# Performance work log

Measured on AMD Instinct MI355X. Metric: run time of the kernel, lower is better.

## Reference

```python
import jax, jax.numpy as jnp
import numpy as np


def setup_inputs() -> dict:
    key = jax.random.key(0)
    k1, k2 = jax.random.split(key)
    queries = jax.random.normal(k1, (8, 4096, 512), dtype=jnp.float32)
    items = jax.random.normal(k2, (1024, 512), dtype=jnp.float32)
    return {"queries": queries, "items": items}


def reference(queries, items):
    # queries: (B, S, F), items: (K, F); reduction='none', memto_framework=True
    # Phase-only (unit magnitude) reconstruction along the sequence axis.
    f = jnp.fft.rfft(queries, axis=1)                     # (B, S//2+1, F) complex64
    unit = jnp.fft.irfft(jnp.exp(-1j * jnp.angle(f)), axis=1)  # (B, S, F) float32 (S even)
    # Dense score against shared memory, then top-1 nearest memory item.
    score = jnp.einsum('bsf,kf->bsk', unit, items)        # (B, S, K)
    idx = jnp.argmax(score, axis=-1)                      # (B, S) int, top-1 index
    step_basis = items[idx]                               # gather -> (B, S, F)
    # MSE with reduction='none' is elementwise squared error; then sum over features.
    gathering_loss = jnp.sum((queries - step_basis) ** 2, axis=-1)  # (B, S)
    return gathering_loss
```

## Files before the change

### kernel.cpp

```cpp
#include <hip/hip_runtime.h>


#define NB 8
#define NS 4096
#define NF 512
#define NK 1024
#define NROWS (NB * NS)
#define NKB 8
#define KK 1024

#define SWZF(i) ((i) ^ (((i) >> 4) & 15))

typedef _Float16 half8 __attribute__((ext_vector_type(8)));
typedef float floatx4 __attribute__((ext_vector_type(4)));
struct H2 { _Float16 x, y; };

__device__ __forceinline__ float2 cmulf(float2 a, float2 b) {
    return make_float2(a.x * b.x - a.y * b.y, a.x * b.y + a.y * b.x);
}

__device__ __forceinline__ float2 unitize(float2 v) {
    float m2 = v.x * v.x + v.y * v.y;
    if (m2 > 0.f) {
        float inv = 1.0f / sqrtf(m2);
        return make_float2(v.x * inv, v.y * inv);
    }
    return make_float2(1.f, 0.f);
}

__device__ __forceinline__ H2 split_h2(float v) {
    _Float16 h = (_Float16)v;
    float lo = v - (float)h;
    H2 r; r.x = h; r.y = (_Float16)lo; return r;
}

__device__ __forceinline__ void dft4(float2 a, float2 b, float2 c, float2 d,
                                     float2& o0, float2& o1, float2& o2, float2& o3) {
    float2 apc = make_float2(a.x + c.x, a.y + c.y);
    float2 amc = make_float2(a.x - c.x, a.y - c.y);
    float2 bpd = make_float2(b.x + d.x, b.y + d.y);
    float2 bmd = make_float2(b.x - d.x, b.y - d.y);
    o0 = make_float2(apc.x + bpd.x, apc.y + bpd.y);
    o1 = make_float2(amc.x + bmd.y, amc.y - bmd.x);
    o2 = make_float2(apc.x - bpd.x, apc.y - bpd.y);
    o3 = make_float2(amc.x - bmd.y, amc.y + bmd.x);
}

__global__ void twiddle_init(float2* __restrict__ W) {
    int k = blockIdx.x * 256 + threadIdx.x;
    double ang = -2.0 * 3.14159265358979323846 * (double)k / 4096.0;
    W[k] = make_float2((float)cos(ang), (float)sin(ang));
}

__global__ __launch_bounds__(256) void transpose_kernel(
        const float* __restrict__ q, float* __restrict__ qt) {
    __shared__ float tile[32][33];
    int b = blockIdx.z;
    int s0 = blockIdx.x * 32;
    int f0 = blockIdx.y * 32;
    int tx = threadIdx.x;
    int ty = threadIdx.y;
    const float* qb = q + (size_t)b * NS * NF;
    float* qtb = qt + (size_t)b * NF * NS;
#pragma unroll
    for (int i = 0; i < 4; ++i) {
        int s = s0 + ty + i * 8;
        tile[ty + i * 8][tx] = qb[(size_t)s * NF + f0 + tx];
    }
    __syncthreads();
#pragma unroll
    for (int i = 0; i < 4; ++i) {
        int f = f0 + ty + i * 8;
        qtb[(size_t)f * NS + s0 + tx] = tile[tx][ty + i * 8];
    }
}

__device__ __forceinline__ void fft4096_r16(float2* A, float2* B,
                                            const float2* __restrict__ W, int t) {
    const float C1 = 0.92387953251128674f;
    const float S1 = 0.38268343236508978f;
    const float R2 = 0.70710678118654752f;
    const float2 w1 = make_float2(C1, -S1);
    const float2 w2 = make_float2(R2, -R2);
    const float2 w3 = make_float2(S1, -C1);
    const float2 w4 = make_float2(0.f, -1.f);
    const float2 w6 = make_float2(-R2, -R2);
    const float2 w9 = make_float2(-C1, S1);
#pragma unroll
    for (int st = 0; st < 3; ++st) {
        float2* src = (st == 1) ? B : A;
        float2* dst = (st == 1) ? A : B;
        const int s = (st == 0) ? 1 : (st == 1) ? 16 : 256;
        __syncthreads();
        float2 x[16];
#pragma unroll
        for (int j = 0; j < 16; ++j) x[j] = src[SWZF(t + j * 256)];
        float2 y[4][4];
#pragma unroll
        for (int n0 = 0; n0 < 4; ++n0)
            dft4(x[n0], x[4 + n0], x[8 + n0], x[12 + n0],
                 y[n0][0], y[n0][1], y[n0][2], y[n0][3]);
        y[1][1] = cmulf(w1, y[1][1]);
        y[1][2] = cmulf(w2, y[1][2]);
        y[1][3] = cmulf(w3, y[1][3]);
        y[2][1] = cmulf(w2, y[2][1]);
        y[2][2] = cmulf(w4, y[2][2]);
        y[2][3] = cmulf(w6, y[2][3]);
        y[3][1] = cmulf(w3, y[3][1]);
        y[3][2] = cmulf(w6, y[3][2]);
        y[3][3] = cmulf(w9, y[3][3]);
        float2 z[16];
#pragma unroll
        for (int k0 = 0; k0 < 4; ++k0)
            dft4(y[0][k0], y[1][k0], y[2][k0], y[3][k0],
                 z[k0], z[4 + k0], z[8 + k0], z[12 + k0]);
        const int q = t & (s - 1);
        const int pw = t - q;
        const int dbase = 16 * t - 15 * q;
        dst[SWZF(dbase)] = z[0];
        if (st == 2) {
#pragma unroll
            for (int j = 1; j < 16; ++j)
                dst[SWZF(dbase + j * s)] = z[j];
        } else {
#pragma unroll
            for (int j = 1; j < 16; ++j)
                dst[SWZF(dbase + j * s)] = cmulf(W[(j * pw) & 4095], z[j]);
        }
    }
}

__global__ __launch_bounds__(256) void fft_phase_kernel(
        const float* __restrict__ qt, H2* __restrict__ u2,
        const float2* __restrict__ W) {
    __shared__ float2 bufA[4096];
    __shared__ float2 bufB[4096];
    const int t = threadIdx.x;
    const float* x0 = qt + (size_t)(2 * blockIdx.x) * NS;
    const float* x1 = x0 + NS;

    const float4* a4 = (const float4*)x0;
    const float4* b4 = (const float4*)x1;
#pragma unroll
    for (int i = 0; i < 4; ++i) {
        int idx = t + i * 256;
        float4 va = a4[idx];
        float4 vb = b4[idx];
        bufA[SWZF(idx * 4 + 0)] = make_float2(va.x, vb.x);
        bufA[SWZF(idx * 4 + 1)] = make_float2(va.y, vb.y);
        bufA[SWZF(idx * 4 + 2)] = make_float2(va.z, vb.z);
        bufA[SWZF(idx * 4 + 3)] = make_float2(va.w, vb.w);
    }

    fft4096_r16(bufA, bufB, W, t);
    __syncthreads();

#pragma unroll
    for (int j = 0; j < 8; ++j) {
        int k = t + j * 256;
        if (k == 0) {
            float2 z0 = bufB[SWZF(0)];
            float2 zh = bufB[SWZF(2048)];
            float2 u00 = unitize(make_float2(z0.x, 0.f));
            float2 u10 = unitize(make_float2(z0.y, 0.f));
            bufB[SWZF(0)] = make_float2(u00.x, u10.x);
            float2 u0h = unitize(make_float2(zh.x, 0.f));
            float2 u1h = unitize(make_float2(zh.y, 0.f));
            bufB[SWZF(2048)] = make_float2(u0h.x, u1h.x);
        } else {
            float2 zk = bufB[SWZF(k)];
            float2 zm = bufB[SWZF(4096 - k)];
            float2 a = make_float2(0.5f * (zk.x + zm.x), 0.5f * (zk.y - zm.y));
            float2 bq = make_float2(0.5f * (zk.x - zm.x), 0.5f * (zk.y + zm.y));
            float2 x1k = make_float2(bq.y, -bq.x);
            float2 u0 = unitize(a);
            float2 u1 = unitize(x1k);
            bufB[SWZF(k)] = make_float2(u0.x - u1.y, u0.y + u1.x);
            bufB[SWZF(4096 - k)] = make_float2(u0.x + u1.y, u1.x - u0.y);
        }
    }

    fft4096_r16(bufB, bufA, W, t);
    __syncthreads();

    H2* o0 = u2 + (size_t)(2 * blockIdx.x) * NS;
    H2* o1 = o0 + NS;
    const float c = 0.25f;
#pragma unroll
    for (int i = 0; i < 4; ++i) {
        int idx = t + i * 256;
        H2 t0[4], t1[4];
#pragma unroll
        for (int k = 0; k < 4; ++k) {
            float2 e = bufA[SWZF(idx * 4 + k)];
            t0[k] = split_h2(e.x * c);
            t1[k] = split_h2(e.y * c);
        }
        *(float4*)&o0[idx * 4] = *(float4*)t0;
        *(float4*)&o1[idx * 4] = *(float4*)t1;
    }
}

__global__ __launch_bounds__(256) void abuild_kernel(
        const H2* __restrict__ u2, _Float16* __restrict__ a2) {
    __shared__ H2 tile[64][65];
    const int b = blockIdx.z;
    const int f0 = blockIdx.y * 64;
    const int s0 = blockIdx.x * 64;
    const int t = threadIdx.x;
    const int fr = t >> 6;
    const int sc = t & 63;
#pragma unroll
    for (int i = 0; i < 16; ++i) {
        int f = fr + i * 4;
        tile[f][sc] = u2[(size_t)(b * NF + f0 + f) * NS + s0 + sc];
    }
    __syncthreads();
    const int s = t >> 2;
    const int qd = t & 3;
    _Float16 xs[16], ys[16];
#pragma unroll
    for (int j = 0; j < 16; ++j) {
        H2 v = tile[qd * 16 + j][s];
        xs[j] = v.x;
        ys[j] = v.y;
    }
    size_t rowoff = ((size_t)(b * NS + s0 + s)) * KK;
    _Float16* pr = a2 + rowoff + (f0 + qd * 16);
    *(float4*)&pr[0] = ((float4*)xs)[0];
    *(float4*)&pr[8] = ((float4*)xs)[1];
    _Float16* pl = pr + 512;
    *(float4*)&pl[0] = ((float4*)ys)[0];
    *(float4*)&pl[8] = ((float4*)ys)[1];
}

__global__ __launch_bounds__(256) void bbuild_kernel(
        const float* __restrict__ items, _Float16* __restrict__ b2) {
    int id = blockIdx.x * 256 + threadIdx.x;
    int n = id >> 7, fq = id & 127;
    float4 v = *(const float4*)&items[(size_t)n * NF + fq * 4];
    H2 h0 = split_h2(v.x * 1024.f);
    H2 h1 = split_h2(v.y * 1024.f);
    H2 h2v = split_h2(v.z * 1024.f);
    H2 h3 = split_h2(v.w * 1024.f);
    _Float16 hs[4] = {h0.x, h1.x, h2v.x, h3.x};
    _Float16 ls[4] = {h0.y, h1.y, h2v.y, h3.y};
    _Float16* pr = b2 + (size_t)n * KK + fq * 4;
    *(float2*)pr = *(float2*)hs;
    *(float2*)(pr + 512) = *(float2*)ls;
}

__global__ __launch_bounds__(256, 2) void gemm_mfma_argmax(
        const _Float16* __restrict__ a2, const _Float16* __restrict__ b2,
        float* __restrict__ pbest, int* __restrict__ pidx) {
    __shared__ __align__(16) char smem[2 * 4 * 128 * 64];
    const int sb = blockIdx.x;
    const int kb = blockIdx.y;
    const int row0 = sb * 128;
    const int n0 = kb * 128;
    const int t = threadIdx.x;
    const int wid = t >> 6, l = t & 63, g = l >> 4, c = l & 15;
    const int wr = wid >> 1, wc = wid & 1;

    floatx4 acc[4][4];
#pragma unroll
    for (int m = 0; m < 4; ++m)
#pragma unroll
        for (int n = 0; n < 4; ++n) acc[m][n] = (floatx4)0.f;

    const int r = t >> 1, h = t & 1;
    const _Float16* gA = a2 + (size_t)(row0 + r) * KK + h * 16;
    const _Float16* gB = b2 + (size_t)(n0 + r) * KK + h * 16;
    const int fsw = (r >> 1) & 3;
    const int w0 = r * 64 + (((2 * h + 0) ^ fsw) << 4);
    const int w1 = r * 64 + (((2 * h + 1) ^ fsw) << 4);

#define TILE(buf, tl) (smem + (size_t)((buf) * 4 + (tl)) * 128 * 64)

    float4 rAh0, rAh1, rAl0, rAl1, rBh0, rBh1, rBl0, rBl1;
#define LOADCH(ch)                                                          \
    {                                                                       \
        const _Float16* pa = gA + (ch) * 32;                                \
        rAh0 = *(const float4*)(pa);                                        \
        rAh1 = *(const float4*)(pa + 8);                                    \
        rAl0 = *(const float4*)(pa + 512);                                  \
        rAl1 = *(const float4*)(pa + 520);                                  \
        const _Float16* pb = gB + (ch) * 32;                                \
        rBh0 = *(const float4*)(pb);                                        \
        rBh1 = *(const float4*)(pb + 8);                                    \
        rBl0 = *(const float4*)(pb + 512);                                  \
        rBl1 = *(const float4*)(pb + 520);                                  \
    }

    LOADCH(0);
    int cur = 0;
    for (int ch = 0; ch < 16; ++ch) {
        *(float4*)(TILE(cur, 0) + w0) = rAh0;
        *(float4*)(TILE(cur, 0) + w1) = rAh1;
        *(float4*)(TILE(cur, 1) + w0) = rAl0;
        *(float4*)(TILE(cur, 1) + w1) = rAl1;
        *(float4*)(TILE(cur, 2) + w0) = rBh0;
        *(float4*)(TILE(cur, 2) + w1) = rBh1;
        *(float4*)(TILE(cur, 3) + w0) = rBl0;
        *(float4*)(TILE(cur, 3) + w1) = rBl1;
        __syncthreads();
        if (ch < 15) LOADCH(ch + 1);
        {
            const char* Ah = TILE(cur, 0);
            const char* Al = TILE(cur, 1);
            const char* Bh = TILE(cur, 2);
            const char* Bl = TILE(cur, 3);
            half8 afh[4], afl[4], bfh[4], bfl[4];
#pragma unroll
            for (int m = 0; m < 4; ++m) {
                int rr = wr * 64 + m * 16 + c;
                int ro = rr * 64 + (((g ^ ((rr >> 1) & 3))) << 4);
                afh[m] = *(const half8*)(Ah + ro);
                afl[m] = *(const half8*)(Al + ro);
            }
#pragma unroll
            for (int n = 0; n < 4; ++n) {
                int rr = wc * 64 + n * 16 + c;
                int ro = rr * 64 + (((g ^ ((rr >> 1) & 3))) << 4);
                bfh[n] = *(const half8*)(Bh + ro);
                bfl[n] = *(const half8*)(Bl + ro);
            }
#pragma unroll
            for (int m = 0; m < 4; ++m)
#pragma unroll
                for (int n = 0; n < 4; ++n) {
                    acc[m][n] = __builtin_amdgcn_mfma_f32_16x16x32_f16(
                        afh[m], bfh[n], acc[m][n], 0, 0, 0);
                    acc[m][n] = __builtin_amdgcn_mfma_f32_16x16x32_f16(
                        afl[m], bfh[n], acc[m][n], 0, 0, 0);
                    acc[m][n] = __builtin_amdgcn_mfma_f32_16x16x32_f16(
                        afh[m], bfl[n], acc[m][n], 0, 0, 0);
                }
        }
        cur ^= 1;
    }
#undef LOADCH
#undef TILE

    __syncthreads();
    float* cand = (float*)smem;
    int* candi = (int*)(smem + 1024);

#pragma unroll
    for (int m = 0; m < 4; ++m) {
#pragma unroll
        for (int rr = 0; rr < 4; ++rr) {
            float best = acc[m][0][rr];
            int bi = c;
#pragma unroll
            for (int n = 1; n < 4; ++n) {
                float v = acc[m][n][rr];
                int ig = n * 16 + c;
                if (v > best) { best = v; bi = ig; }
            }
#pragma unroll
            for (int off = 1; off < 16; off <<= 1) {
                float ov = __shfl_xor(best, off);
                int oi = __shfl_xor(bi, off);
                if (ov > best || (ov == best && oi < bi)) { best = ov; bi = oi; }
            }
            if (c == 0) {
                int s_local = wr * 64 + m * 16 + 4 * g + rr;
                cand[wc * 128 + s_local] = best;
                candi[wc * 128 + s_local] = bi;
            }
        }
    }
    __syncthreads();
    if (t < 128) {
        float b0v = cand[t];
        int b0i = candi[t];
        float b1v = cand[128 + t];
        int b1i = candi[128 + t] + 64;
        float best = b0v; int bi = b0i;
        if (b1v > b0v) { best = b1v; bi = b1i; }
        int row = row0 + t;
        pbest[(size_t)row * NKB + kb] = best;
        pidx[(size_t)row * NKB + kb] = n0 + bi;
    }
}

__global__ __launch_bounds__(256) void combine_loss_kernel(
        const float* __restrict__ q, const float* __restrict__ items,
        const float* __restrict__ pbest, const int* __restrict__ pidx,
        float* __restrict__ out) {
    const int wid = threadIdx.x >> 6;
    const int lane = threadIdx.x & 63;
    const int row = blockIdx.x * 4 + wid;

    float best = pbest[(size_t)row * NKB];
    int bidx = pidx[(size_t)row * NKB];
#pragma unroll
    for (int g = 1; g < NKB; ++g) {
        float v = pbest[(size_t)row * NKB + g];
        if (v > best) { best = v; bidx = pidx[(size_t)row * NKB + g]; }
    }

    const float4* qr = (const float4*)(q + (size_t)row * NF);
    const float4* mr = (const float4*)(items + (size_t)bidx * NF);
    float sum = 0.f;
#pragma unroll
    for (int i = 0; i < 2; ++i) {
        float4 a = qr[lane + i * 64];
        float4 m = mr[lane + i * 64];
        float dx = a.x - m.x, dy = a.y - m.y, dz = a.z - m.z, dw = a.w - m.w;
        sum += dx * dx + dy * dy + dz * dz + dw * dw;
    }
#pragma unroll
    for (int off = 32; off; off >>= 1) sum += __shfl_down(sum, off, 64);
    if (lane == 0) out[row] = sum;
}

extern "C" void kernel_launch(void* const* d_in, const int* in_sizes, int n_in,
                              void* d_out, int out_size, void* d_ws, size_t ws_size,
                              hipStream_t stream) {
    const float* q = (const float*)d_in[0];
    const float* items = (const float*)d_in[1];
    float* out = (float*)d_out;

    char* ws = (char*)d_ws;
    float2* W = (float2*)ws;
    float* qt = (float*)(ws + 32768);
    _Float16* a2 = (_Float16*)(ws + 32768);
    H2* u2 = (H2*)(ws + 32768 + (size_t)67108864);
    _Float16* b2 = (_Float16*)(ws + 32768 + (size_t)67108864 * 2);
    float* pbest = (float*)(ws + 32768 + (size_t)67108864 * 2 + 2097152);
    int* pidx = (int*)(ws + 32768 + (size_t)67108864 * 2 + 2097152 + 1048576);

    hipLaunchKernelGGL(twiddle_init, dim3(16), dim3(256), 0, stream, W);
    hipLaunchKernelGGL(transpose_kernel, dim3(128, 16, 8), dim3(32, 8, 1), 0,
                       stream, q, qt);
    hipLaunchKernelGGL(fft_phase_kernel, dim3(2048), dim3(256), 0, stream,
                       qt, u2, W);
    hipLaunchKernelGGL(abuild_kernel, dim3(64, 8, 8), dim3(256), 0, stream,
                       u2, a2);
    hipLaunchKernelGGL(bbuild_kernel, dim3(512), dim3(256), 0, stream,
                       items, b2);
    hipLaunchKernelGGL(gemm_mfma_argmax, dim3(256, 8), dim3(256), 0, stream,
                       a2, b2, pbest, pidx);
    hipLaunchKernelGGL(combine_loss_kernel, dim3(NROWS / 4), dim3(256), 0,
                       stream, q, items, pbest, pidx, out);
}
```

Before: 320.2 us.

## Pre-swizzle GEMM operands into MFMA fragment layout and load directly from global

The A and B build kernels now write the split-fp16 operands in a blocked layout that matches the MFMA 16x16x32 fragment order, so each lane reads a contiguous half8 straight from global memory. The GEMM drops its LDS staging, its double-buffered tiles and the per-chunk barriers, and instead keeps register-level double buffering of fragments. This removes LDS traffic and synchronisation, but operand data is no longer shared through LDS across the waves of a block, so global/L2 load traffic per block rises and more registers are held live.

```diff
diff --git a/kernel.cpp b/kernel.cpp
--- a/kernel.cpp
+++ b/kernel.cpp
@@ -202,7 +202,7 @@
 }
 
 __global__ __launch_bounds__(256) void abuild_kernel(
-        const H2* __restrict__ u2, _Float16* __restrict__ a2) {
+        const H2* __restrict__ u2, _Float16* __restrict__ a3) {
     __shared__ H2 tile[64][65];
     const int b = blockIdx.z;
     const int f0 = blockIdx.y * 64;
@@ -225,35 +225,44 @@
         xs[j] = v.x;
         ys[j] = v.y;
     }
-    size_t rowoff = ((size_t)(b * NS + s0 + s)) * KK;
-    _Float16* pr = a2 + rowoff + (f0 + qd * 16);
-    *(float4*)&pr[0] = ((float4*)xs)[0];
-    *(float4*)&pr[8] = ((float4*)xs)[1];
-    _Float16* pl = pr + 512;
-    *(float4*)&pl[0] = ((float4*)ys)[0];
-    *(float4*)&pl[8] = ((float4*)ys)[1];
+    const int f = f0 + qd * 16;
+    const int s_g = b * NS + s0 + s;
+    const int rb = s_g >> 4;
+    const int sl = s_g & 15;
+    const int kc = f >> 5;
+    const int g0 = (f >> 3) & 3;
+    size_t base = ((size_t)rb * 32 + kc) * 512;
+    *(float4*)(a3 + base + (g0 * 16 + sl) * 8) = ((float4*)xs)[0];
+    *(float4*)(a3 + base + ((g0 + 1) * 16 + sl) * 8) = ((float4*)xs)[1];
+    base += 16 * 512;
+    *(float4*)(a3 + base + (g0 * 16 + sl) * 8) = ((float4*)ys)[0];
+    *(float4*)(a3 + base + ((g0 + 1) * 16 + sl) * 8) = ((float4*)ys)[1];
 }
 
 __global__ __launch_bounds__(256) void bbuild_kernel(
-        const float* __restrict__ items, _Float16* __restrict__ b2) {
+        const float* __restrict__ items, _Float16* __restrict__ b3) {
     int id = blockIdx.x * 256 + threadIdx.x;
     int n = id >> 7, fq = id & 127;
-    float4 v = *(const float4*)&items[(size_t)n * NF + fq * 4];
+    int f = fq * 4;
+    float4 v = *(const float4*)&items[(size_t)n * NF + f];
     H2 h0 = split_h2(v.x * 1024.f);
     H2 h1 = split_h2(v.y * 1024.f);
     H2 h2v = split_h2(v.z * 1024.f);
     H2 h3 = split_h2(v.w * 1024.f);
     _Float16 hs[4] = {h0.x, h1.x, h2v.x, h3.x};
     _Float16 ls[4] = {h0.y, h1.y, h2v.y, h3.y};
-    _Float16* pr = b2 + (size_t)n * KK + fq * 4;
-    *(float2*)pr = *(float2*)hs;
-    *(float2*)(pr + 512) = *(float2*)ls;
+    const int rb = n >> 4, nl = n & 15;
+    const int kc = f >> 5, g = (f >> 3) & 3, off = f & 7;
+    size_t base = ((size_t)rb * 32 + kc) * 512 + (g * 16 + nl) * 8 + off;
+    *(float2*)(b3 + base) = *(float2*)hs;
+    *(float2*)(b3 + base + 16 * 512) = *(float2*)ls;
 }
 
 __global__ __launch_bounds__(256, 2) void gemm_mfma_argmax(
-        const _Float16* __restrict__ a2, const _Float16* __restrict__ b2,
+        const _Float16* __restrict__ a3, const _Float16* __restrict__ b3,
         float* __restrict__ pbest, int* __restrict__ pidx) {
-    __shared__ __align__(16) char smem[2 * 4 * 128 * 64];
+    __shared__ float smemf[256];
+    __shared__ int smemi[256];
     const int sb = blockIdx.x;
     const int kb = blockIdx.y;
     const int row0 = sb * 128;
@@ -268,83 +277,46 @@
 #pragma unroll
         for (int n = 0; n < 4; ++n) acc[m][n] = (floatx4)0.f;
 
-    const int r = t >> 1, h = t & 1;
-    const _Float16* gA = a2 + (size_t)(row0 + r) * KK + h * 16;
-    const _Float16* gB = b2 + (size_t)(n0 + r) * KK + h * 16;
-    const int fsw = (r >> 1) & 3;
-    const int w0 = r * 64 + (((2 * h + 0) ^ fsw) << 4);
-    const int w1 = r * 64 + (((2 * h + 1) ^ fsw) << 4);
-
-#define TILE(buf, tl) (smem + (size_t)((buf) * 4 + (tl)) * 128 * 64)
-
-    float4 rAh0, rAh1, rAl0, rAl1, rBh0, rBh1, rBl0, rBl1;
-#define LOADCH(ch)                                                          \
+    const _Float16* pa = a3 + ((size_t)(sb * 8 + wr * 4) * 32) * 512 + l * 8;
+    const _Float16* pb = b3 + ((size_t)(kb * 8 + wc * 4) * 32) * 512 + l * 8;
+
+    half8 cah[4], cal[4], cbh[4], cbl[4];
+    half8 nah[4], nal[4], nbh[4], nbl[4];
+
+#define LOADF(ah, al, bh, bl, ch)                                           \
     {                                                                       \
-        const _Float16* pa = gA + (ch) * 32;                                \
-        rAh0 = *(const float4*)(pa);                                        \
-        rAh1 = *(const float4*)(pa + 8);                                    \
-        rAl0 = *(const float4*)(pa + 512);                                  \
-        rAl1 = *(const float4*)(pa + 520);                                  \
-        const _Float16* pb = gB + (ch) * 32;                                \
-        rBh0 = *(const float4*)(pb);                                        \
-        rBh1 = *(const float4*)(pb + 8);                                    \
-        rBl0 = *(const float4*)(pb + 512);                                  \
-        rBl1 = *(const float4*)(pb + 520);                                  \
-    }
-
-    LOADCH(0);
-    int cur = 0;
-    for (int ch = 0; ch < 16; ++ch) {
-        *(float4*)(TILE(cur, 0) + w0) = rAh0;
-        *(float4*)(TILE(cur, 0) + w1) = rAh1;
-        *(float4*)(TILE(cur, 1) + w0) = rAl0;
-        *(float4*)(TILE(cur, 1) + w1) = rAl1;
-        *(float4*)(TILE(cur, 2) + w0) = rBh0;
-        *(float4*)(TILE(cur, 2) + w1) = rBh1;
-        *(float4*)(TILE(cur, 3) + w0) = rBl0;
-        *(float4*)(TILE(cur, 3) + w1) = rBl1;
-        __syncthreads();
-        if (ch < 15) LOADCH(ch + 1);
-        {
-            const char* Ah = TILE(cur, 0);
-            const char* Al = TILE(cur, 1);
-            const char* Bh = TILE(cur, 2);
-            const char* Bl = TILE(cur, 3);
-            half8 afh[4], afl[4], bfh[4], bfl[4];
-#pragma unroll
-            for (int m = 0; m < 4; ++m) {
-                int rr = wr * 64 + m * 16 + c;
-                int ro = rr * 64 + (((g ^ ((rr >> 1) & 3))) << 4);
-                afh[m] = *(const half8*)(Ah + ro);
-                afl[m] = *(const half8*)(Al + ro);
-            }
-#pragma unroll
-            for (int n = 0; n < 4; ++n) {
-                int rr = wc * 64 + n * 16 + c;
-                int ro = rr * 64 + (((g ^ ((rr >> 1) & 3))) << 4);
-                bfh[n] = *(const half8*)(Bh + ro);
-                bfl[n] = *(const half8*)(Bl + ro);
-            }
-#pragma unroll
-            for (int m = 0; m < 4; ++m)
-#pragma unroll
-                for (int n = 0; n < 4; ++n) {
-                    acc[m][n] = __builtin_amdgcn_mfma_f32_16x16x32_f16(
-                        afh[m], bfh[n], acc[m][n], 0, 0, 0);
-                    acc[m][n] = __builtin_amdgcn_mfma_f32_16x16x32_f16(
-                        afl[m], bfh[n], acc[m][n], 0, 0, 0);
-                    acc[m][n] = __builtin_amdgcn_mfma_f32_16x16x32_f16(
-                        afh[m], bfl[n], acc[m][n], 0, 0, 0);
-                }
-        }
-        cur ^= 1;
-    }
-#undef LOADCH
-#undef TILE
-
-    __syncthreads();
-    float* cand = (float*)smem;
-    int* candi = (int*)(smem + 1024);
+        _Pragma("unroll") for (int m = 0; m < 4; ++m) {                     \
+            ah[m] = *(const half8*)(pa + m * 16384 + (ch) * 512);           \
+            al[m] = *(const half8*)(pa + m * 16384 + (16 + (ch)) * 512);    \
+        }                                                                   \
+        _Pragma("unroll") for (int n = 0; n < 4; ++n) {                     \
+            bh[n] = *(const half8*)(pb + n * 16384 + (ch) * 512);           \
+            bl[n] = *(const half8*)(pb + n * 16384 + (16 + (ch)) * 512);    \
+        }                                                                   \
+    }
+
+#define MFMAS(ah, al, bh, bl)                                               \
+    {                                                                       \
+        _Pragma("unroll") for (int m = 0; m < 4; ++m)                       \
+        _Pragma("unroll") for (int n = 0; n < 4; ++n) {                     \
+            acc[m][n] = __builtin_amdgcn_mfma_f32_16x16x32_f16(             \
+                ah[m], bh[n], acc[m][n], 0, 0, 0);                          \
+            acc[m][n] = __builtin_amdgcn_mfma_f32_16x16x32_f16(             \
+                al[m], bh[n], acc[m][n], 0, 0, 0);                          \
+            acc[m][n] = __builtin_amdgcn_mfma_f32_16x16x32_f16(             \
+                ah[m], bl[n], acc[m][n], 0, 0, 0);                          \
+        }                                                                   \
+    }
+
+    LOADF(cah, cal, cbh, cbl, 0);
+    for (int c0 = 0; c0 < 16; c0 += 2) {
+        if (c0 + 1 < 16) LOADF(nah, nal, nbh, nbl, c0 + 1);
+        MFMAS(cah, cal, cbh, cbl);
+        if (c0 + 2 < 16) LOADF(cah, cal, cbh, cbl, c0 + 2);
+        MFMAS(nah, nal, nbh, nbl);
+    }
+#undef LOADF
+#undef MFMAS
 
 #pragma unroll
     for (int m = 0; m < 4; ++m) {
@@ -366,17 +338,17 @@
             }
             if (c == 0) {
                 int s_local = wr * 64 + m * 16 + 4 * g + rr;
-                cand[wc * 128 + s_local] = best;
-                candi[wc * 128 + s_local] = bi;
+                smemf[wc * 128 + s_local] = best;
+                smemi[wc * 128 + s_local] = bi;
             }
         }
     }
     __syncthreads();
     if (t < 128) {
-        float b0v = cand[t];
-        int b0i = candi[t];
-        float b1v = cand[128 + t];
-        int b1i = candi[128 + t] + 64;
+        float b0v = smemf[t];
+        int b0i = smemi[t];
+        float b1v = smemf[128 + t];
+        int b1i = smemi[128 + t] + 64;
         float best = b0v; int bi = b0i;
         if (b1v > b0v) { best = b1v; bi = b1i; }
         int row = row0 + t;
@@ -426,9 +398,9 @@
     char* ws = (char*)d_ws;
     float2* W = (float2*)ws;
     float* qt = (float*)(ws + 32768);
-    _Float16* a2 = (_Float16*)(ws + 32768);
+    _Float16* a3 = (_Float16*)(ws + 32768);
     H2* u2 = (H2*)(ws + 32768 + (size_t)67108864);
-    _Float16* b2 = (_Float16*)(ws + 32768 + (size_t)67108864 * 2);
+    _Float16* b3 = (_Float16*)(ws + 32768 + (size_t)67108864 * 2);
     float* pbest = (float*)(ws + 32768 + (size_t)67108864 * 2 + 2097152);
     int* pidx = (int*)(ws + 32768 + (size_t)67108864 * 2 + 2097152 + 1048576);
 
@@ -438,11 +410,11 @@
     hipLaunchKernelGGL(fft_phase_kernel, dim3(2048), dim3(256), 0, stream,
                        qt, u2, W);
     hipLaunchKernelGGL(abuild_kernel, dim3(64, 8, 8), dim3(256), 0, stream,
-                       u2, a2);
+                       u2, a3);
     hipLaunchKernelGGL(bbuild_kernel, dim3(512), dim3(256), 0, stream,
-                       items, b2);
+                       items, b3);
     hipLaunchKernelGGL(gemm_mfma_argmax, dim3(256, 8), dim3(256), 0, stream,
-                       a2, b2, pbest, pidx);
+                       a3, b3, pbest, pidx);
     hipLaunchKernelGGL(combine_loss_kernel, dim3(NROWS / 4), dim3(256), 0,
                        stream, q, items, pbest, pidx, out);
 }
```

Result: no change. 314.2 us (-1.9%).
